# Kernel optimization log

Hardware: AMD Instinct MI355X
Metric: run time of the kernel (lower is better)

## Reference

```python
import jax, jax.numpy as jnp
import numpy as np

N = 100000


def seg_mean(feat, src, dst, n):
    # gather at src, scatter-mean at dst (PyG mean aggr: 0 for isolated nodes)
    s = jax.ops.segment_sum(feat[src], dst, num_segments=n)
    cnt = jax.ops.segment_sum(jnp.ones((src.shape[0],), feat.dtype), dst, num_segments=n)
    return s / jnp.maximum(cnt, 1.0)[:, None]


def setup_inputs() -> dict:
    key = jax.random.key(0)
    ks = jax.random.split(key, 8)
    d_in, d_h = 64, 32
    E = 1_250_000
    inp = {
        "x": jax.random.normal(ks[0], (N, d_in), jnp.float32),
        "W1_pos": jax.random.normal(ks[1], (2 * d_in, d_h), jnp.float32) * 0.05,
        "b1_pos": jnp.zeros((d_h,), jnp.float32),
        "W1_neg": jax.random.normal(ks[2], (2 * d_in, d_h), jnp.float32) * 0.05,
        "b1_neg": jnp.zeros((d_h,), jnp.float32),
        "W2_pos": jax.random.normal(ks[3], (3 * d_h, d_h), jnp.float32) * 0.05,
        "b2_pos": jnp.zeros((d_h,), jnp.float32),
        "W2_neg": jax.random.normal(ks[4], (3 * d_h, d_h), jnp.float32) * 0.05,
        "b2_neg": jnp.zeros((d_h,), jnp.float32),
        "pos_edge_index": jax.random.randint(ks[5], (2, E), 0, N, jnp.int64),
        "neg_edge_index": jax.random.randint(ks[6], (2, E), 0, N, jnp.int64),
    }
    return inp


def reference(x, W1_pos, b1_pos, W1_neg, b1_neg, W2_pos, b2_pos, W2_neg, b2_neg,
              pos_edge_index, neg_edge_index):
    ps, pd = pos_edge_index[0], pos_edge_index[1]
    ns, nd = neg_edge_index[0], neg_edge_index[1]
    n = x.shape[0]

    # --- layer 1 (first_aggr=True) ---
    ap = seg_mean(x, ps, pd, n)          # [N, 64]
    an = seg_mean(x, ns, nd, n)
    out_p = jnp.concatenate([ap, x], -1) @ W1_pos + b1_pos   # [N, 32]
    out_n = jnp.concatenate([an, x], -1) @ W1_neg + b1_neg
    z = jnp.tanh(jnp.concatenate([out_p, out_n], -1))        # [N, 64]

    # --- layer 2 (first_aggr=False) ---
    d_h = out_p.shape[-1]
    zp, zn = z[:, :d_h], z[:, d_h:]
    out_p = jnp.concatenate([seg_mean(zp, ps, pd, n), seg_mean(zn, ns, nd, n), zp], -1) @ W2_pos + b2_pos
    out_n = jnp.concatenate([seg_mean(zn, ps, pd, n), seg_mean(zp, ns, nd, n), zn], -1) @ W2_neg + b2_neg
    z = jnp.tanh(jnp.concatenate([out_p, out_n], -1))
    return z
```

## Files before the change

### kernel.cpp

```cpp
#include <hip/hip_runtime.h>
#include <math.h>


typedef _Float16 h4 __attribute__((ext_vector_type(4)));
typedef _Float16 h8 __attribute__((ext_vector_type(8)));
typedef float f32x4 __attribute__((ext_vector_type(4)));

__device__ inline h8 shflx8(h8 v, int m) {
    int4 i = __builtin_bit_cast(int4, v);
    i.x = __shfl_xor(i.x, m);
    i.y = __shfl_xor(i.y, m);
    i.z = __shfl_xor(i.z, m);
    i.w = __shfl_xor(i.w, m);
    return __builtin_bit_cast(h8, i);
}

__device__ inline float fast_tanh(float v) {
    float e = __expf(2.0f * v);
    return 1.0f - 2.0f / (e + 1.0f);
}


#define BSHIFT 9
#define BSIZE  512
#define NBMAX  512
#define NREP   8
#define RCAP   1024
#define CAP    (NREP * RCAP)
#define MAXPER 4992


__device__ inline float b1map(const float* W1p, const float* W1n, int k, int c)
{
    if (c < 32) {
        if (k < 64)   return W1p[k * 32 + c];
        if (k >= 128) return W1p[(k - 64) * 32 + c];
        return 0.0f;
    } else {
        int cn = c - 32;
        if (k >= 64)  return W1n[(k - 64) * 32 + cn];
        return 0.0f;
    }
}

__device__ inline float b2map(const float* W2p, const float* W2n, int k, int c)
{
    if (c < 32) {
        if (k < 32)               return W2p[k * 32 + c];
        if (k >= 96 && k < 128)   return W2p[(k - 96 + 32) * 32 + c];
        if (k >= 128 && k < 160)  return W2p[(k - 128 + 64) * 32 + c];
        return 0.0f;
    } else {
        int cn = c - 32;
        if (k >= 32 && k < 64)    return W2n[(k - 32) * 32 + cn];
        if (k >= 64 && k < 96)    return W2n[(k - 64 + 32) * 32 + cn];
        if (k >= 160)             return W2n[(k - 160 + 64) * 32 + cn];
        return 0.0f;
    }
}


__global__ void __launch_bounds__(256) mega_k(
    const int* __restrict__ pos, const int* __restrict__ neg,
    int* __restrict__ pcntR, unsigned* __restrict__ ebuf,
    int E, int n, int nb, int bblocks,
    const float4* __restrict__ x, h4* __restrict__ xh, int n4, int cvtBlocks,
    const float* __restrict__ W1p, const float* __restrict__ W1n,
    const float* __restrict__ W2p, const float* __restrict__ W2n,
    _Float16* __restrict__ Bpack)
{
    int tid = threadIdx.x;
    int bid = blockIdx.x;

    if (bid >= bblocks) {
        int cb = bid - bblocks;
        if (cb < cvtBlocks) {
            int gs = cvtBlocks * 256;
            for (int i = cb * 256 + tid; i < n4; i += gs) {
                float4 v = x[i];
                h4 o = { (_Float16)v.x, (_Float16)v.y, (_Float16)v.z, (_Float16)v.w };
                xh[i] = o;
            }
        } else {
            int slot = (cb - cvtBlocks) * 256 + tid;
            if (slot < 2 * 24 * 64) {
                int mat  = slot / (24 * 64);
                int rem  = slot % (24 * 64);
                int fg   = rem / 64;
                int lane = rem % 64;
                int kk = fg >> 2, nt = fg & 3;
                int g = lane >> 4, m = lane & 15;
                _Float16* dst = Bpack + (size_t)slot * 8;
                int c = nt * 16 + m;
                #pragma unroll
                for (int j = 0; j < 8; ++j) {
                    int k = kk * 32 + g * 8 + j;
                    float v = mat ? b2map(W2p, W2n, k, c) : b1map(W1p, W1n, k, c);
                    dst[j] = (_Float16)v;
                }
            }
        }
        return;
    }

    __shared__ int cnt[NBMAX], gbase[NBMAX], lofs[NBMAX], sc2[256];
    __shared__ unsigned erec[MAXPER], sorted[MAXPER];
    __shared__ unsigned short ep[MAXPER], pd[MAXPER];
    int rep = bid & (NREP - 1);
    int per = (2 * E + bblocks - 1) / bblocks;
    int e0 = bid * per;
    int e1 = min(e0 + per, 2 * E);
    int cntloc = e1 - e0;

    for (int i = tid; i < nb; i += 256) cnt[i] = 0;
    __syncthreads();

    for (int e = e0 + tid; e < e1; e += 256) {
        int nd, sr;
        if (e < E) { nd = pos[E + e];                 sr = pos[e]; }
        else       { int ee = e - E; nd = n + neg[E + ee]; sr = neg[ee]; }
        int p = nd >> BSHIFT;
        int li = e - e0;
        erec[li] = ((unsigned)(nd & (BSIZE - 1)) << 17) | (unsigned)sr;
        ep[li] = (unsigned short)p;
        atomicAdd(&cnt[p], 1);
    }
    __syncthreads();
    for (int i = tid; i < nb; i += 256) {
        int c = cnt[i];
        gbase[i] = c ? atomicAdd(&pcntR[rep * NBMAX + i], c) : 0;
    }
    {
        int a0 = (2 * tid     < nb) ? cnt[2 * tid]     : 0;
        int a1 = (2 * tid + 1 < nb) ? cnt[2 * tid + 1] : 0;
        int s = a0 + a1;
        sc2[tid] = s;
        __syncthreads();
        for (int off = 1; off < 256; off <<= 1) {
            int t = (tid >= off) ? sc2[tid - off] : 0;
            __syncthreads();
            sc2[tid] += t;
            __syncthreads();
        }
        int excl = sc2[tid] - s;
        if (2 * tid     < nb) lofs[2 * tid]     = excl;
        if (2 * tid + 1 < nb) lofs[2 * tid + 1] = excl + a0;
    }
    __syncthreads();
    for (int i = tid; i < nb; i += 256) cnt[i] = 0;
    __syncthreads();
    for (int li = tid; li < cntloc; li += 256) {
        int p = ep[li];
        int r = atomicAdd(&cnt[p], 1);
        int idx = lofs[p] + r;
        sorted[idx] = erec[li];
        pd[idx] = (unsigned short)p;
    }
    __syncthreads();
    for (int t = tid; t < cntloc; t += 256) {
        int p = pd[t];
        int g = gbase[p] + (t - lofs[p]);
        if (g < RCAP)
            ebuf[(size_t)p * CAP + rep * RCAP + g] = sorted[t];
    }
}

__global__ void __launch_bounds__(1024) scatter_k(
    const unsigned* __restrict__ ebuf, const int* __restrict__ pcntR,
    int* __restrict__ cur, int* __restrict__ col, int n, int nb)
{
    __shared__ int lcnt[BSIZE], lbase[BSIZE], sc[256], bb[NBMAX], crp[NREP];
    __shared__ int lcol[CAP];
    int p = blockIdx.x;
    int tid = threadIdx.x;
    int n2 = 2 * n;
    int lo = p << BSHIFT;
    int nn = min(BSIZE, n2 - lo);
    const unsigned* bbuf = ebuf + (size_t)p * CAP;

    if (tid < NREP) crp[tid] = min(pcntR[tid * NBMAX + p], RCAP);

    {
        int a0 = 0, a1 = 0, s = 0;
        if (tid < 256) {
            #pragma unroll
            for (int r = 0; r < NREP; ++r) {
                if (2 * tid     < nb) a0 += min(pcntR[r * NBMAX + 2 * tid],     RCAP);
                if (2 * tid + 1 < nb) a1 += min(pcntR[r * NBMAX + 2 * tid + 1], RCAP);
            }
            s = a0 + a1;
            sc[tid] = s;
        }
        __syncthreads();
        for (int off = 1; off < 256; off <<= 1) {
            int t = (tid < 256 && tid >= off) ? sc[tid - off] : 0;
            __syncthreads();
            if (tid < 256) sc[tid] += t;
            __syncthreads();
        }
        if (tid < 256) {
            int excl = sc[tid] - s;
            bb[2 * tid]     = excl;
            bb[2 * tid + 1] = excl + a0;
        }
    }

    for (int i = tid; i < BSIZE; i += 1024) lcnt[i] = 0;
    __syncthreads();
    int cnttot = crp[0] + crp[1] + crp[2] + crp[3] +
                 crp[4] + crp[5] + crp[6] + crp[7];
    #pragma unroll
    for (int r = 0; r < NREP; ++r) {
        int c = crp[r];
        const unsigned* buf = bbuf + r * RCAP;
        for (int i = tid; i < c; i += 1024)
            atomicAdd(&lcnt[buf[i] >> 17], 1);
    }
    __syncthreads();
    {
        int a0 = 0, a1 = 0, s = 0;
        if (tid < 256) {
            a0 = lcnt[2 * tid]; a1 = lcnt[2 * tid + 1];
            s = a0 + a1;
            sc[tid] = s;
        }
        __syncthreads();
        for (int off = 1; off < 256; off <<= 1) {
            int t = (tid < 256 && tid >= off) ? sc[tid - off] : 0;
            __syncthreads();
            if (tid < 256) sc[tid] += t;
            __syncthreads();
        }
        if (tid < 256) {
            int excl = sc[tid] - s;
            lbase[2 * tid]     = excl;
            lbase[2 * tid + 1] = excl + a0;
        }
    }
    __syncthreads();
    int gb = bb[p];
    for (int i = tid; i < nn; i += 1024)
        cur[lo + i] = gb + lbase[i] + lcnt[i];
    __syncthreads();
    #pragma unroll
    for (int r = 0; r < NREP; ++r) {
        int c = crp[r];
        const unsigned* buf = bbuf + r * RCAP;
        for (int i = tid; i < c; i += 1024) {
            unsigned v = buf[i];
            int slot = atomicAdd(&lbase[v >> 17], 1);
            lcol[slot] = (int)(v & 0x1FFFFu);
        }
    }
    __syncthreads();
    for (int t = tid; t < cnttot; t += 1024)
        col[gb + t] = lcol[t];
}


__global__ void __launch_bounds__(256) agg_k(
    const h8* __restrict__ feat8,
    const int* __restrict__ cur, const int* __restrict__ col,
    h8* __restrict__ ag8, int n)
{
    int tid = threadIdx.x;
    int wave = tid >> 6, lane = tid & 63;
    int s = lane >> 2, f = lane & 3;
    int list = s >> 3;
    int sub = s & 7;

    int stride = gridDim.x * 4;
    for (int node = blockIdx.x * 4 + wave; node < n; node += stride) {
        int idx = list ? n + node : node;
        int r0 = idx ? cur[idx - 1] : 0;
        int r1 = cur[idx];

        h8 acc0 = {}, acc1 = {};
        #pragma unroll 2
        for (int it = r0 + sub; it < r1; it += 8) {
            unsigned srcb = (unsigned)col[it] * 8;
            acc0 = acc0 + feat8[srcb + f];
            acc1 = acc1 + feat8[srcb + 4 + f];
        }
        acc0 = acc0 + shflx8(acc0, 4);
        acc1 = acc1 + shflx8(acc1, 4);
        acc0 = acc0 + shflx8(acc0, 8);
        acc1 = acc1 + shflx8(acc1, 8);
        acc0 = acc0 + shflx8(acc0, 16);
        acc1 = acc1 + shflx8(acc1, 16);
        _Float16 inv = (_Float16)(1.0f / (float)max(r1 - r0, 1));
        h8 iv = { inv, inv, inv, inv, inv, inv, inv, inv };
        if (sub == 0) {
            ag8[(unsigned)(node * 16 + list * 8 + f)]     = acc0 * iv;
            ag8[(unsigned)(node * 16 + list * 8 + 4 + f)] = acc1 * iv;
        }
    }
}


#define ROWP 200

__device__ inline int nmap(int g, int r) {
    return 32 * (16 * (g >> 3) + (r >> 2)) + 4 * (g & 7) + (r & 3);
}

__global__ void __launch_bounds__(256) gemm_k(
    const h8* __restrict__ ag8, const h8* __restrict__ feat8,
    const h8* __restrict__ Bp,
    const float* __restrict__ bp, const float* __restrict__ bn,
    float* __restrict__ outf, _Float16* __restrict__ outh,
    int f32out, int n)
{
    __shared__ _Float16 A_lds[64 * ROWP];
    int tid = threadIdx.x;
    int bid = blockIdx.x;

    for (int ch = tid; ch < 64 * 24; ch += 256) {
        int r = ch / 24, p = ch % 24;
        int row = min(nmap(bid, r), n - 1);
        h8 v = (p < 16) ? ag8[(size_t)row * 16 + p]
                        : feat8[(size_t)row * 8 + (p - 16)];
        *(h8*)&A_lds[r * ROWP + p * 8] = v;
    }
    __syncthreads();

    int w = tid >> 6, lane = tid & 63;
    int m = lane & 15, g = lane >> 4;

    h8 a[6];
    #pragma unroll
    for (int kk = 0; kk < 6; ++kk)
        a[kk] = *(const h8*)&A_lds[(w * 16 + m) * ROWP + kk * 32 + g * 8];

    #pragma unroll
    for (int nt = 0; nt < 4; ++nt) {
        f32x4 acc = { 0.f, 0.f, 0.f, 0.f };
        #pragma unroll
        for (int kk = 0; kk < 6; ++kk) {
            h8 b = Bp[(kk * 4 + nt) * 64 + lane];
            acc = __builtin_amdgcn_mfma_f32_16x16x32_f16(a[kk], b, acc, 0, 0, 0);
        }
        int colc = nt * 16 + m;
        float bias = (colc < 32) ? bp[colc] : bn[colc - 32];
        #pragma unroll
        for (int reg = 0; reg < 4; ++reg) {
            int node = nmap(bid, w * 16 + g * 4 + reg);
            if (node < n) {
                float val = fast_tanh(acc[reg] + bias);
                if (f32out) outf[(size_t)node * 64 + colc] = val;
                else        outh[(size_t)node * 64 + colc] = (_Float16)val;
            }
        }
    }
}

extern "C" void kernel_launch(void* const* d_in, const int* in_sizes, int n_in,
                              void* d_out, int out_size, void* d_ws, size_t ws_size,
                              hipStream_t stream)
{
    const float* x   = (const float*)d_in[0];
    const float* W1p = (const float*)d_in[1];
    const float* b1p = (const float*)d_in[2];
    const float* W1n = (const float*)d_in[3];
    const float* b1n = (const float*)d_in[4];
    const float* W2p = (const float*)d_in[5];
    const float* b2p = (const float*)d_in[6];
    const float* W2n = (const float*)d_in[7];
    const float* b2n = (const float*)d_in[8];
    const int*   pos = (const int*)d_in[9];
    const int*   neg = (const int*)d_in[10];

    int n = in_sizes[0] / 64;
    int E = in_sizes[9] / 2;
    int n2 = 2 * n;
    int nb = (n2 + BSIZE - 1) / BSIZE;

    int*      pcntR = (int*)d_ws;
    int*      cur   = pcntR + NREP * NBMAX;
    int*      col   = cur + n2;
    _Float16* Bpack = (_Float16*)(col + 2 * (size_t)E);
    _Float16* xh    = Bpack + 2 * 24 * 64 * 8;
    unsigned* ebuf  = (unsigned*)(xh + (size_t)n * 64);
    _Float16* zh    = (_Float16*)ebuf;
    h8*       ag8   = (h8*)d_out;

    hipMemsetAsync(pcntR, 0, NREP * NBMAX * sizeof(int), stream);

    int bblocks = 512;
    int n4 = n * 16;
    int cvtBlocks = 512;

    mega_k<<<bblocks + cvtBlocks + 12, 256, 0, stream>>>(
        pos, neg, pcntR, ebuf, E, n, nb, bblocks,
        (const float4*)x, (h4*)xh, n4, cvtBlocks,
        W1p, W1n, W2p, W2n, Bpack);

    scatter_k<<<nb, 1024, 0, stream>>>(ebuf, pcntR, cur, col, n, nb);

    int ablocks = 2048;
    int gblocks = (n + 63) / 64 + 5;

    agg_k <<<ablocks, 256, 0, stream>>>((const h8*)xh, cur, col, ag8, n);
    gemm_k<<<gblocks, 256, 0, stream>>>(ag8, (const h8*)xh, (const h8*)Bpack,
                                        b1p, b1n, nullptr, zh, 0, n);

    agg_k <<<ablocks, 256, 0, stream>>>((const h8*)zh, cur, col, ag8, n);
    gemm_k<<<gblocks, 256, 0, stream>>>(ag8, (const h8*)zh,
                                        (const h8*)(Bpack + 24 * 64 * 8),
                                        b2p, b2n, (float*)d_out, nullptr, 1, n);
}
```

Baseline: 262.6 us.

## Merge graph build and per-layer agg+GEMM into cooperative persistent kernels

Replaces the memset, bucketing kernel and scatter kernel with one cooperative build kernel that uses grid-wide syncs between phases and processes edges in chunks. Each layer's aggregation and GEMM are merged into one cooperative kernel with a grid sync between them, and the GEMM reads self features straight from global memory instead of staging them in LDS. This removes several launches and the gaps between them. In exchange it adds grid-sync cost, limits the grid to occupancy-bounded persistent blocks, and uses smaller per-block edge chunks. It falls back to the old launch path if a cooperative launch fails.

```diff
diff --git a/kernel.cpp b/kernel.cpp
--- a/kernel.cpp
+++ b/kernel.cpp
@@ -1,6 +1,9 @@
 #include <hip/hip_runtime.h>
+#include <hip/hip_cooperative_groups.h>
 #include <math.h>
 
+
+namespace cg = cooperative_groups;
 
 typedef _Float16 h4 __attribute__((ext_vector_type(4)));
 typedef _Float16 h8 __attribute__((ext_vector_type(8)));
@@ -20,15 +23,14 @@
     return 1.0f - 2.0f / (e + 1.0f);
 }
 
-
 #define BSHIFT 9
 #define BSIZE  512
 #define NBMAX  512
 #define NREP   8
 #define RCAP   1024
 #define CAP    (NREP * RCAP)
-#define MAXPER 4992
-
+#define MAXPER_F 4992
+#define MAXPER_C 2560
 
 __device__ inline float b1map(const float* W1p, const float* W1n, int k, int c)
 {
@@ -56,6 +58,302 @@
         if (k >= 64 && k < 96)    return W2n[(k - 64 + 32) * 32 + cn];
         if (k >= 160)             return W2n[(k - 160 + 64) * 32 + cn];
         return 0.0f;
+    }
+}
+
+__device__ inline int nmap(int g, int r) {
+    return 32 * (16 * (g >> 3) + (r >> 2)) + 4 * (g & 7) + (r & 3);
+}
+
+#define ROWP 200
+
+
+__global__ void __launch_bounds__(256) build_k(
+    const int* __restrict__ pos, const int* __restrict__ neg,
+    int* __restrict__ pcntR, unsigned* __restrict__ ebuf,
+    int E, int n, int nb,
+    const float4* __restrict__ x, h4* __restrict__ xh, int n4,
+    const float* __restrict__ W1p, const float* __restrict__ W1n,
+    const float* __restrict__ W2p, const float* __restrict__ W2n,
+    _Float16* __restrict__ Bpack,
+    int* __restrict__ cur, int* __restrict__ col)
+{
+    __shared__ int lcnt[NBMAX], lgb[NBMAX], sc[256], bb[NBMAX], crp[NREP];
+    __shared__ int lcol[CAP / 2];
+    __shared__ int lcol2[CAP / 2];
+    unsigned* erec = (unsigned*)lcol;
+    unsigned* sorted = erec + MAXPER_C;
+    unsigned short* ep = (unsigned short*)(sorted + MAXPER_C);
+    unsigned short* pd = ep + MAXPER_C;
+
+    cg::grid_group grid = cg::this_grid();
+    int tid = threadIdx.x;
+    int bid = blockIdx.x;
+    int g = gridDim.x;
+    int n2 = 2 * n;
+
+    for (int i = bid * 256 + tid; i < NREP * NBMAX; i += g * 256)
+        pcntR[i] = 0;
+    grid.sync();
+
+    {
+        int rep = bid & (NREP - 1);
+        int per = (2 * E + g - 1) / g;
+        int e0 = bid * per;
+        int e1 = min(e0 + per, 2 * E);
+        for (int c0 = e0; c0 < e1; c0 += MAXPER_C) {
+            int c1 = min(c0 + MAXPER_C, e1);
+            int cl = c1 - c0;
+            for (int i = tid; i < nb; i += 256) lcnt[i] = 0;
+            __syncthreads();
+            for (int e = c0 + tid; e < c1; e += 256) {
+                int nd, sr;
+                if (e < E) { nd = pos[E + e];                 sr = pos[e]; }
+                else       { int ee = e - E; nd = n + neg[E + ee]; sr = neg[ee]; }
+                int p = nd >> BSHIFT;
+                int li = e - c0;
+                erec[li] = ((unsigned)(nd & (BSIZE - 1)) << 17) | (unsigned)sr;
+                ep[li] = (unsigned short)p;
+                atomicAdd(&lcnt[p], 1);
+            }
+            __syncthreads();
+            for (int i = tid; i < nb; i += 256) {
+                int c = lcnt[i];
+                lgb[i] = c ? atomicAdd(&pcntR[rep * NBMAX + i], c) : 0;
+            }
+            {
+                int a0 = (2 * tid     < nb) ? lcnt[2 * tid]     : 0;
+                int a1 = (2 * tid + 1 < nb) ? lcnt[2 * tid + 1] : 0;
+                int s = a0 + a1;
+                sc[tid] = s;
+                __syncthreads();
+                for (int off = 1; off < 256; off <<= 1) {
+                    int t = (tid >= off) ? sc[tid - off] : 0;
+                    __syncthreads();
+                    sc[tid] += t;
+                    __syncthreads();
+                }
+                int excl = sc[tid] - s;
+                if (2 * tid     < nb) bb[2 * tid]     = excl;
+                if (2 * tid + 1 < nb) bb[2 * tid + 1] = excl + a0;
+            }
+            __syncthreads();
+            for (int i = tid; i < nb; i += 256) lcnt[i] = 0;
+            __syncthreads();
+            for (int li = tid; li < cl; li += 256) {
+                int p = ep[li];
+                int r = atomicAdd(&lcnt[p], 1);
+                int idx = bb[p] + r;
+                sorted[idx] = erec[li];
+                pd[idx] = (unsigned short)p;
+            }
+            __syncthreads();
+            for (int t = tid; t < cl; t += 256) {
+                int p = pd[t];
+                int gg = lgb[p] + (t - bb[p]);
+                if (gg < RCAP)
+                    ebuf[(size_t)p * CAP + rep * RCAP + gg] = sorted[t];
+            }
+            __syncthreads();
+        }
+    }
+    grid.sync();
+
+    {
+        int a0 = 0, a1 = 0, s = 0;
+        #pragma unroll
+        for (int r = 0; r < NREP; ++r) {
+            if (2 * tid     < nb) a0 += min(pcntR[r * NBMAX + 2 * tid],     RCAP);
+            if (2 * tid + 1 < nb) a1 += min(pcntR[r * NBMAX + 2 * tid + 1], RCAP);
+        }
+        s = a0 + a1;
+        sc[tid] = s;
+        __syncthreads();
+        for (int off = 1; off < 256; off <<= 1) {
+            int t = (tid >= off) ? sc[tid - off] : 0;
+            __syncthreads();
+            sc[tid] += t;
+            __syncthreads();
+        }
+        int excl = sc[tid] - s;
+        if (2 * tid     < nb) bb[2 * tid]     = excl;
+        if (2 * tid + 1 < nb) bb[2 * tid + 1] = excl + a0;
+    }
+    __syncthreads();
+
+    int ncvt = (n4 + 4095) / 4096;
+    int ntask = nb + 12 + ncvt;
+    for (int task = bid; task < ntask; task += g) {
+        if (task < nb) {
+            int p = task;
+            int lo = p << BSHIFT;
+            int nn = min(BSIZE, n2 - lo);
+            const unsigned* bbuf = ebuf + (size_t)p * CAP;
+            __syncthreads();
+            if (tid < NREP) crp[tid] = min(pcntR[tid * NBMAX + p], RCAP);
+            for (int i = tid; i < BSIZE; i += 256) lcnt[i] = 0;
+            __syncthreads();
+            int cnttot = 0;
+            #pragma unroll
+            for (int r = 0; r < NREP; ++r) {
+                int c = crp[r];
+                cnttot += c;
+                const unsigned* buf = bbuf + r * RCAP;
+                for (int i = tid; i < c; i += 256)
+                    atomicAdd(&lcnt[buf[i] >> 17], 1);
+            }
+            __syncthreads();
+            {
+                int a0 = lcnt[2 * tid], a1 = lcnt[2 * tid + 1];
+                int s = a0 + a1;
+                sc[tid] = s;
+                __syncthreads();
+                for (int off = 1; off < 256; off <<= 1) {
+                    int t = (tid >= off) ? sc[tid - off] : 0;
+                    __syncthreads();
+                    sc[tid] += t;
+                    __syncthreads();
+                }
+                int excl = sc[tid] - s;
+                lgb[2 * tid]     = excl;
+                lgb[2 * tid + 1] = excl + a0;
+            }
+            __syncthreads();
+            int gb = bb[p];
+            for (int i = tid; i < nn; i += 256)
+                cur[lo + i] = gb + lgb[i] + lcnt[i];
+            __syncthreads();
+            int* lc = lcol;
+            #pragma unroll
+            for (int r = 0; r < NREP; ++r) {
+                int c = crp[r];
+                const unsigned* buf = bbuf + r * RCAP;
+                for (int i = tid; i < c; i += 256) {
+                    unsigned v = buf[i];
+                    int slot = atomicAdd(&lgb[v >> 17], 1);
+                    if (slot < CAP / 2) lc[slot] = (int)(v & 0x1FFFFu);
+                    else                lcol2[slot - CAP / 2] = (int)(v & 0x1FFFFu);
+                }
+            }
+            __syncthreads();
+            for (int t = tid; t < cnttot; t += 256)
+                col[gb + t] = (t < CAP / 2) ? lc[t] : lcol2[t - CAP / 2];
+            __syncthreads();
+        } else if (task < nb + 12) {
+            int slot = (task - nb) * 256 + tid;
+            if (slot < 2 * 24 * 64) {
+                int mat  = slot / (24 * 64);
+                int rem  = slot % (24 * 64);
+                int fg   = rem / 64;
+                int lane = rem % 64;
+                int kk = fg >> 2, nt = fg & 3;
+                int gq = lane >> 4, m = lane & 15;
+                _Float16* dst = Bpack + (size_t)slot * 8;
+                int c = nt * 16 + m;
+                #pragma unroll
+                for (int j = 0; j < 8; ++j) {
+                    int k = kk * 32 + gq * 8 + j;
+                    float v = mat ? b2map(W2p, W2n, k, c) : b1map(W1p, W1n, k, c);
+                    dst[j] = (_Float16)v;
+                }
+            }
+        } else {
+            int ct = task - nb - 12;
+            int i0 = ct * 4096;
+            int i1 = min(i0 + 4096, n4);
+            for (int i = i0 + tid; i < i1; i += 256) {
+                float4 v = x[i];
+                h4 o = { (_Float16)v.x, (_Float16)v.y, (_Float16)v.z, (_Float16)v.w };
+                xh[i] = o;
+            }
+        }
+    }
+}
+
+__global__ void __launch_bounds__(256, 8) layer_k(
+    const h8* __restrict__ feat8,
+    const int* __restrict__ cur, const int* __restrict__ col,
+    const h8* __restrict__ Bp,
+    const float* __restrict__ bp, const float* __restrict__ bn,
+    h8* __restrict__ ag8, float* __restrict__ outf, _Float16* __restrict__ outh,
+    int f32out, int n, int ntiles)
+{
+    __shared__ _Float16 A_lds[64 * 132];
+    cg::grid_group gridg = cg::this_grid();
+    int tid = threadIdx.x;
+    int wave = tid >> 6, lane = tid & 63;
+
+    {
+        int s = lane >> 2, f = lane & 3;
+        int list = s >> 3;
+        int sub = s & 7;
+        int stride = gridDim.x * 4;
+        for (int node = blockIdx.x * 4 + wave; node < n; node += stride) {
+            int idx = list ? n + node : node;
+            int r0 = idx ? cur[idx - 1] : 0;
+            int r1 = cur[idx];
+            h8 acc0 = {}, acc1 = {};
+            #pragma unroll 2
+            for (int it = r0 + sub; it < r1; it += 8) {
+                unsigned srcb = (unsigned)col[it] * 8;
+                acc0 = acc0 + feat8[srcb + f];
+                acc1 = acc1 + feat8[srcb + 4 + f];
+            }
+            acc0 = acc0 + shflx8(acc0, 4);
+            acc1 = acc1 + shflx8(acc1, 4);
+            acc0 = acc0 + shflx8(acc0, 8);
+            acc1 = acc1 + shflx8(acc1, 8);
+            acc0 = acc0 + shflx8(acc0, 16);
+            acc1 = acc1 + shflx8(acc1, 16);
+            _Float16 inv = (_Float16)(1.0f / (float)max(r1 - r0, 1));
+            h8 iv = { inv, inv, inv, inv, inv, inv, inv, inv };
+            if (sub == 0) {
+                ag8[(unsigned)(node * 16 + list * 8 + f)]     = acc0 * iv;
+                ag8[(unsigned)(node * 16 + list * 8 + 4 + f)] = acc1 * iv;
+            }
+        }
+    }
+    gridg.sync();
+
+    int w = wave;
+    int m = lane & 15, g4 = lane >> 4;
+    for (int t = blockIdx.x; t < ntiles; t += gridDim.x) {
+        __syncthreads();
+        for (int ch = tid; ch < 64 * 16; ch += 256) {
+            int r = ch >> 4, c = ch & 15;
+            int row = min(nmap(t, r), n - 1);
+            *(h8*)&A_lds[r * 132 + c * 8] = ag8[(size_t)row * 16 + c];
+        }
+        __syncthreads();
+
+        int rowm = min(nmap(t, w * 16 + m), n - 1);
+        h8 a[6];
+        #pragma unroll
+        for (int kk = 0; kk < 4; ++kk)
+            a[kk] = *(const h8*)&A_lds[(w * 16 + m) * 132 + kk * 32 + g4 * 8];
+        a[4] = feat8[(size_t)rowm * 8 + g4];
+        a[5] = feat8[(size_t)rowm * 8 + 4 + g4];
+
+        #pragma unroll
+        for (int nt = 0; nt < 4; ++nt) {
+            f32x4 acc = { 0.f, 0.f, 0.f, 0.f };
+            #pragma unroll
+            for (int kk = 0; kk < 6; ++kk) {
+                h8 b = Bp[(kk * 4 + nt) * 64 + lane];
+                acc = __builtin_amdgcn_mfma_f32_16x16x32_f16(a[kk], b, acc, 0, 0, 0);
+            }
+            int colc = nt * 16 + m;
+            float bias = (colc < 32) ? bp[colc] : bn[colc - 32];
+            #pragma unroll
+            for (int reg = 0; reg < 4; ++reg) {
+                int node = nmap(t, w * 16 + g4 * 4 + reg);
+                if (node < n) {
+                    float val = fast_tanh(acc[reg] + bias);
+                    if (f32out) outf[(size_t)node * 64 + colc] = val;
+                    else        outh[(size_t)node * 64 + colc] = (_Float16)val;
+                }
+            }
+        }
     }
 }
 
@@ -104,8 +402,8 @@
     }
 
     __shared__ int cnt[NBMAX], gbase[NBMAX], lofs[NBMAX], sc2[256];
-    __shared__ unsigned erec[MAXPER], sorted[MAXPER];
-    __shared__ unsigned short ep[MAXPER], pd[MAXPER];
+    __shared__ unsigned erec[MAXPER_F], sorted[MAXPER_F];
+    __shared__ unsigned short ep[MAXPER_F], pd[MAXPER_F];
     int rep = bid & (NREP - 1);
     int per = (2 * E + bblocks - 1) / bblocks;
     int e0 = bid * per;
@@ -114,7 +412,6 @@
 
     for (int i = tid; i < nb; i += 256) cnt[i] = 0;
     __syncthreads();
-
     for (int e = e0 + tid; e < e1; e += 256) {
         int nd, sr;
         if (e < E) { nd = pos[E + e];                 sr = pos[e]; }
@@ -179,7 +476,6 @@
     const unsigned* bbuf = ebuf + (size_t)p * CAP;
 
     if (tid < NREP) crp[tid] = min(pcntR[tid * NBMAX + p], RCAP);
-
     {
         int a0 = 0, a1 = 0, s = 0;
         if (tid < 256) {
@@ -204,7 +500,6 @@
             bb[2 * tid + 1] = excl + a0;
         }
     }
-
     for (int i = tid; i < BSIZE; i += 1024) lcnt[i] = 0;
     __syncthreads();
     int cnttot = crp[0] + crp[1] + crp[2] + crp[3] +
@@ -257,7 +552,6 @@
         col[gb + t] = lcol[t];
 }
 
-
 __global__ void __launch_bounds__(256) agg_k(
     const h8* __restrict__ feat8,
     const int* __restrict__ cur, const int* __restrict__ col,
@@ -268,13 +562,11 @@
     int s = lane >> 2, f = lane & 3;
     int list = s >> 3;
     int sub = s & 7;
-
     int stride = gridDim.x * 4;
     for (int node = blockIdx.x * 4 + wave; node < n; node += stride) {
         int idx = list ? n + node : node;
         int r0 = idx ? cur[idx - 1] : 0;
         int r1 = cur[idx];
-
         h8 acc0 = {}, acc1 = {};
         #pragma unroll 2
         for (int it = r0 + sub; it < r1; it += 8) {
@@ -297,13 +589,6 @@
     }
 }
 
-
-#define ROWP 200
-
-__device__ inline int nmap(int g, int r) {
-    return 32 * (16 * (g >> 3) + (r >> 2)) + 4 * (g & 7) + (r & 3);
-}
-
 __global__ void __launch_bounds__(256) gemm_k(
     const h8* __restrict__ ag8, const h8* __restrict__ feat8,
     const h8* __restrict__ Bp,
@@ -314,7 +599,6 @@
     __shared__ _Float16 A_lds[64 * ROWP];
     int tid = threadIdx.x;
     int bid = blockIdx.x;
-
     for (int ch = tid; ch < 64 * 24; ch += 256) {
         int r = ch / 24, p = ch % 24;
         int row = min(nmap(bid, r), n - 1);
@@ -323,15 +607,12 @@
         *(h8*)&A_lds[r * ROWP + p * 8] = v;
     }
     __syncthreads();
-
     int w = tid >> 6, lane = tid & 63;
     int m = lane & 15, g = lane >> 4;
-
     h8 a[6];
     #pragma unroll
     for (int kk = 0; kk < 6; ++kk)
         a[kk] = *(const h8*)&A_lds[(w * 16 + m) * ROWP + kk * 32 + g * 8];
-
     #pragma unroll
     for (int nt = 0; nt < 4; ++nt) {
         f32x4 acc = { 0.f, 0.f, 0.f, 0.f };
@@ -353,6 +634,7 @@
         }
     }
 }
+
 
 extern "C" void kernel_launch(void* const* d_in, const int* in_sizes, int n_in,
                               void* d_out, int out_size, void* d_ws, size_t ws_size,
@@ -384,28 +666,87 @@
     _Float16* zh    = (_Float16*)ebuf;
     h8*       ag8   = (h8*)d_out;
 
+    int n4 = n * 16;
+    int ntiles = ((n + 511) / 512) * 8;
+
+    bool coop = true;
+    int occB = 0, occL = 0;
+    if (hipOccupancyMaxActiveBlocksPerMultiprocessor(&occB, build_k, 256, 0) != hipSuccess ||
+        hipOccupancyMaxActiveBlocksPerMultiprocessor(&occL, layer_k, 256, 0) != hipSuccess ||
+        occB < 1 || occL < 1)
+        coop = false;
+
+    if (coop) {
+        int gB = min(1024, occB * 256);
+        int gL = min(2048, occL * 256);
+        const float4* x4 = (const float4*)x;
+        h4* xh4 = (h4*)xh;
+        void* bargs[] = { (void*)&pos, (void*)&neg, (void*)&pcntR, (void*)&ebuf,
+                          (void*)&E, (void*)&n, (void*)&nb,
+                          (void*)&x4, (void*)&xh4, (void*)&n4,
+                          (void*)&W1p, (void*)&W1n, (void*)&W2p, (void*)&W2n,
+                          (void*)&Bpack, (void*)&cur, (void*)&col };
+        if (hipLaunchCooperativeKernel(build_k, dim3(gB), dim3(256),
+                                       bargs, 0, stream) != hipSuccess) {
+            (void)hipGetLastError();
+            coop = false;
+        } else {
+            const h8* f1 = (const h8*)xh;
+            const h8* Bp1 = (const h8*)Bpack;
+            float* nof = nullptr;
+            _Float16* zh_ = zh;
+            int zero = 0, one = 1;
+            void* l1[] = { (void*)&f1, (void*)&cur, (void*)&col, (void*)&Bp1,
+                           (void*)&b1p, (void*)&b1n, (void*)&ag8,
+                           (void*)&nof, (void*)&zh_, (void*)&zero,
+                           (void*)&n, (void*)&ntiles };
+            if (hipLaunchCooperativeKernel(layer_k, dim3(gL), dim3(256),
+                                           l1, 0, stream) != hipSuccess) {
+                (void)hipGetLastError();
+                coop = false;
+            } else {
+                const h8* f2 = (const h8*)zh;
+                const h8* Bp2 = (const h8*)(Bpack + 24 * 64 * 8);
+                float* of = (float*)d_out;
+                _Float16* noh = nullptr;
+                void* l2[] = { (void*)&f2, (void*)&cur, (void*)&col, (void*)&Bp2,
+                               (void*)&b2p, (void*)&b2n, (void*)&ag8,
+                               (void*)&of, (void*)&noh, (void*)&one,
+                               (void*)&n, (void*)&ntiles };
+                if (hipLaunchCooperativeKernel(layer_k, dim3(gL), dim3(256),
+                                               l2, 0, stream) == hipSuccess)
+                    return;
+                (void)hipGetLastError();
+                agg_k <<<2048, 256, 0, stream>>>((const h8*)zh, cur, col, ag8, n);
+                gemm_k<<<ntiles, 256, 0, stream>>>(ag8, (const h8*)zh,
+                                                   (const h8*)(Bpack + 24 * 64 * 8),
+                                                   b2p, b2n, (float*)d_out, nullptr, 1, n);
+                return;
+            }
+            agg_k <<<2048, 256, 0, stream>>>((const h8*)xh, cur, col, ag8, n);
+            gemm_k<<<ntiles, 256, 0, stream>>>(ag8, (const h8*)xh, (const h8*)Bpack,
+                                               b1p, b1n, nullptr, zh, 0, n);
+            agg_k <<<2048, 256, 0, stream>>>((const h8*)zh, cur, col, ag8, n);
+            gemm_k<<<ntiles, 256, 0, stream>>>(ag8, (const h8*)zh,
+                                               (const h8*)(Bpack + 24 * 64 * 8),
+                                               b2p, b2n, (float*)d_out, nullptr, 1, n);
+            return;
+        }
+    }
+
     hipMemsetAsync(pcntR, 0, NREP * NBMAX * sizeof(int), stream);
-
     int bblocks = 512;
-    int n4 = n * 16;
     int cvtBlocks = 512;
-
     mega_k<<<bblocks + cvtBlocks + 12, 256, 0, stream>>>(
         pos, neg, pcntR, ebuf, E, n, nb, bblocks,
         (const float4*)x, (h4*)xh, n4, cvtBlocks,
         W1p, W1n, W2p, W2n, Bpack);
-
     scatter_k<<<nb, 1024, 0, stream>>>(ebuf, pcntR, cur, col, n, nb);
-
-    int ablocks = 2048;
-    int gblocks = (n + 63) / 64 + 5;
-
-    agg_k <<<ablocks, 256, 0, stream>>>((const h8*)xh, cur, col, ag8, n);
-    gemm_k<<<gblocks, 256, 0, stream>>>(ag8, (const h8*)xh, (const h8*)Bpack,
-                                        b1p, b1n, nullptr, zh, 0, n);
-
-    agg_k <<<ablocks, 256, 0, stream>>>((const h8*)zh, cur, col, ag8, n);
-    gemm_k<<<gblocks, 256, 0, stream>>>(ag8, (const h8*)zh,
-                                        (const h8*)(Bpack + 24 * 64 * 8),
-                                        b2p, b2n, (float*)d_out, nullptr, 1, n);
-}
+    agg_k <<<2048, 256, 0, stream>>>((const h8*)xh, cur, col, ag8, n);
+    gemm_k<<<ntiles, 256, 0, stream>>>(ag8, (const h8*)xh, (const h8*)Bpack,
+                                       b1p, b1n, nullptr, zh, 0, n);
+    agg_k <<<2048, 256, 0, stream>>>((const h8*)zh, cur, col, ag8, n);
+    gemm_k<<<ntiles, 256, 0, stream>>>(ag8, (const h8*)zh,
+                                       (const h8*)(Bpack + 24 * 64 * 8),
+                                       b2p, b2n, (float*)d_out, nullptr, 1, n);
+}
```

Result: slower. 748.9 us (+185.2%).

## Fuse per-layer aggregation and GEMM into one persistent kernel with grid barrier

Applied to the files above, without the earlier changes.

Merges agg_k and gemm_k into a single layer_k launch per layer. Blocks first do the neighbour-mean aggregation and write results with agent-scope atomic stores, then meet at a global atomic-counter barrier before doing the MFMA GEMM over node tiles in a grid-stride loop. The self-feature half of the A operand is now loaded straight from global memory into registers instead of being staged through LDS. The aim is to cut kernel launches and the gap between them, at the cost of relying on all 1536 blocks being co-resident (launch_bounds 256,7) and a spin-wait barrier that has a timeout fallback.

```diff
diff --git a/kernel.cpp b/kernel.cpp
--- a/kernel.cpp
+++ b/kernel.cpp
@@ -20,7 +20,6 @@
     return 1.0f - 2.0f / (e + 1.0f);
 }
 
-
 #define BSHIFT 9
 #define BSIZE  512
 #define NBMAX  512
@@ -28,7 +27,6 @@
 #define RCAP   1024
 #define CAP    (NREP * RCAP)
 #define MAXPER 4992
-
 
 __device__ inline float b1map(const float* W1p, const float* W1n, int k, int c)
 {
@@ -57,6 +55,10 @@
         if (k >= 160)             return W2n[(k - 160 + 64) * 32 + cn];
         return 0.0f;
     }
+}
+
+__device__ inline int nmap(int g, int r) {
+    return 32 * (16 * (g >> 3) + (r >> 2)) + 4 * (g & 7) + (r & 3);
 }
 
 
@@ -114,7 +116,6 @@
 
     for (int i = tid; i < nb; i += 256) cnt[i] = 0;
     __syncthreads();
-
     for (int e = e0 + tid; e < e1; e += 256) {
         int nd, sr;
         if (e < E) { nd = pos[E + e];                 sr = pos[e]; }
@@ -179,7 +180,6 @@
     const unsigned* bbuf = ebuf + (size_t)p * CAP;
 
     if (tid < NREP) crp[tid] = min(pcntR[tid * NBMAX + p], RCAP);
-
     {
         int a0 = 0, a1 = 0, s = 0;
         if (tid < 256) {
@@ -204,7 +204,6 @@
             bb[2 * tid + 1] = excl + a0;
         }
     }
-
     for (int i = tid; i < BSIZE; i += 1024) lcnt[i] = 0;
     __syncthreads();
     int cnttot = crp[0] + crp[1] + crp[2] + crp[3] +
@@ -258,101 +257,113 @@
 }
 
 
-__global__ void __launch_bounds__(256) agg_k(
+__global__ void __launch_bounds__(256, 7) layer_k(
     const h8* __restrict__ feat8,
     const int* __restrict__ cur, const int* __restrict__ col,
-    h8* __restrict__ ag8, int n)
-{
+    const h8* __restrict__ Bp,
+    const float* __restrict__ bp, const float* __restrict__ bn,
+    unsigned long long* __restrict__ ag64,
+    float* __restrict__ outf, _Float16* __restrict__ outh,
+    int f32out, int n, int ntiles, int* __restrict__ bar, int nblk)
+{
+    __shared__ _Float16 A_lds[64 * 132];
     int tid = threadIdx.x;
     int wave = tid >> 6, lane = tid & 63;
-    int s = lane >> 2, f = lane & 3;
-    int list = s >> 3;
-    int sub = s & 7;
-
-    int stride = gridDim.x * 4;
-    for (int node = blockIdx.x * 4 + wave; node < n; node += stride) {
-        int idx = list ? n + node : node;
-        int r0 = idx ? cur[idx - 1] : 0;
-        int r1 = cur[idx];
-
-        h8 acc0 = {}, acc1 = {};
-        #pragma unroll 2
-        for (int it = r0 + sub; it < r1; it += 8) {
-            unsigned srcb = (unsigned)col[it] * 8;
-            acc0 = acc0 + feat8[srcb + f];
-            acc1 = acc1 + feat8[srcb + 4 + f];
-        }
-        acc0 = acc0 + shflx8(acc0, 4);
-        acc1 = acc1 + shflx8(acc1, 4);
-        acc0 = acc0 + shflx8(acc0, 8);
-        acc1 = acc1 + shflx8(acc1, 8);
-        acc0 = acc0 + shflx8(acc0, 16);
-        acc1 = acc1 + shflx8(acc1, 16);
-        _Float16 inv = (_Float16)(1.0f / (float)max(r1 - r0, 1));
-        h8 iv = { inv, inv, inv, inv, inv, inv, inv, inv };
-        if (sub == 0) {
-            ag8[(unsigned)(node * 16 + list * 8 + f)]     = acc0 * iv;
-            ag8[(unsigned)(node * 16 + list * 8 + 4 + f)] = acc1 * iv;
-        }
-    }
-}
-
-
-#define ROWP 200
-
-__device__ inline int nmap(int g, int r) {
-    return 32 * (16 * (g >> 3) + (r >> 2)) + 4 * (g & 7) + (r & 3);
-}
-
-__global__ void __launch_bounds__(256) gemm_k(
-    const h8* __restrict__ ag8, const h8* __restrict__ feat8,
-    const h8* __restrict__ Bp,
-    const float* __restrict__ bp, const float* __restrict__ bn,
-    float* __restrict__ outf, _Float16* __restrict__ outh,
-    int f32out, int n)
-{
-    __shared__ _Float16 A_lds[64 * ROWP];
-    int tid = threadIdx.x;
-    int bid = blockIdx.x;
-
-    for (int ch = tid; ch < 64 * 24; ch += 256) {
-        int r = ch / 24, p = ch % 24;
-        int row = min(nmap(bid, r), n - 1);
-        h8 v = (p < 16) ? ag8[(size_t)row * 16 + p]
-                        : feat8[(size_t)row * 8 + (p - 16)];
-        *(h8*)&A_lds[r * ROWP + p * 8] = v;
-    }
-    __syncthreads();
-
-    int w = tid >> 6, lane = tid & 63;
-    int m = lane & 15, g = lane >> 4;
-
-    h8 a[6];
-    #pragma unroll
-    for (int kk = 0; kk < 6; ++kk)
-        a[kk] = *(const h8*)&A_lds[(w * 16 + m) * ROWP + kk * 32 + g * 8];
-
-    #pragma unroll
-    for (int nt = 0; nt < 4; ++nt) {
-        f32x4 acc = { 0.f, 0.f, 0.f, 0.f };
+
+    {
+        int s = lane >> 2, f = lane & 3;
+        int list = s >> 3;
+        int sub = s & 7;
+        int stride = gridDim.x * 4;
+        for (int node = blockIdx.x * 4 + wave; node < n; node += stride) {
+            int idx = list ? n + node : node;
+            int r0 = idx ? cur[idx - 1] : 0;
+            int r1 = cur[idx];
+            h8 acc0 = {}, acc1 = {};
+            #pragma unroll 2
+            for (int it = r0 + sub; it < r1; it += 8) {
+                unsigned srcb = (unsigned)col[it] * 8;
+                acc0 = acc0 + feat8[srcb + f];
+                acc1 = acc1 + feat8[srcb + 4 + f];
+            }
+            acc0 = acc0 + shflx8(acc0, 4);
+            acc1 = acc1 + shflx8(acc1, 4);
+            acc0 = acc0 + shflx8(acc0, 8);
+            acc1 = acc1 + shflx8(acc1, 8);
+            acc0 = acc0 + shflx8(acc0, 16);
+            acc1 = acc1 + shflx8(acc1, 16);
+            _Float16 inv = (_Float16)(1.0f / (float)max(r1 - r0, 1));
+            h8 iv = { inv, inv, inv, inv, inv, inv, inv, inv };
+            if (sub == 0) {
+                h8 v0 = acc0 * iv, v1 = acc1 * iv;
+                ulonglong2 u0 = __builtin_bit_cast(ulonglong2, v0);
+                ulonglong2 u1 = __builtin_bit_cast(ulonglong2, v1);
+                size_t b0 = (size_t)(unsigned)(node * 16 + list * 8 + f) * 2;
+                size_t b1 = (size_t)(unsigned)(node * 16 + list * 8 + 4 + f) * 2;
+                __hip_atomic_store(&ag64[b0],     u0.x, __ATOMIC_RELAXED, __HIP_MEMORY_SCOPE_AGENT);
+                __hip_atomic_store(&ag64[b0 + 1], u0.y, __ATOMIC_RELAXED, __HIP_MEMORY_SCOPE_AGENT);
+                __hip_atomic_store(&ag64[b1],     u1.x, __ATOMIC_RELAXED, __HIP_MEMORY_SCOPE_AGENT);
+                __hip_atomic_store(&ag64[b1 + 1], u1.y, __ATOMIC_RELAXED, __HIP_MEMORY_SCOPE_AGENT);
+            }
+        }
+    }
+
+    __syncthreads();
+    if (tid == 0) {
+        __hip_atomic_fetch_add(bar, 1, __ATOMIC_RELEASE, __HIP_MEMORY_SCOPE_AGENT);
+        long spins = 0;
+        while (__hip_atomic_load(bar, __ATOMIC_ACQUIRE, __HIP_MEMORY_SCOPE_AGENT) < nblk) {
+            __builtin_amdgcn_s_sleep(16);
+            if (++spins > (1L << 20)) break;
+        }
+    }
+    __syncthreads();
+
+    int m = lane & 15, g4 = lane >> 4;
+    for (int t = blockIdx.x; t < ntiles; t += gridDim.x) {
+        __syncthreads();
+        for (int ch = tid; ch < 64 * 16; ch += 256) {
+            int r = ch >> 4, c = ch & 15;
+            int row = min(nmap(t, r), n - 1);
+            size_t bi = ((size_t)row * 16 + c) * 2;
+            unsigned long long w0 = __hip_atomic_load(&ag64[bi],     __ATOMIC_RELAXED, __HIP_MEMORY_SCOPE_AGENT);
+            unsigned long long w1 = __hip_atomic_load(&ag64[bi + 1], __ATOMIC_RELAXED, __HIP_MEMORY_SCOPE_AGENT);
+            ulonglong2 u; u.x = w0; u.y = w1;
+            *(h8*)&A_lds[r * 132 + c * 8] = __builtin_bit_cast(h8, u);
+        }
+        __syncthreads();
+
+        int rowm = min(nmap(t, wave * 16 + m), n - 1);
+        h8 a[6];
         #pragma unroll
-        for (int kk = 0; kk < 6; ++kk) {
-            h8 b = Bp[(kk * 4 + nt) * 64 + lane];
-            acc = __builtin_amdgcn_mfma_f32_16x16x32_f16(a[kk], b, acc, 0, 0, 0);
-        }
-        int colc = nt * 16 + m;
-        float bias = (colc < 32) ? bp[colc] : bn[colc - 32];
+        for (int kk = 0; kk < 4; ++kk)
+            a[kk] = *(const h8*)&A_lds[(wave * 16 + m) * 132 + kk * 32 + g4 * 8];
+        a[4] = feat8[(size_t)rowm * 8 + g4];
+        a[5] = feat8[(size_t)rowm * 8 + 4 + g4];
+
         #pragma unroll
-        for (int reg = 0; reg < 4; ++reg) {
-            int node = nmap(bid, w * 16 + g * 4 + reg);
-            if (node < n) {
-                float val = fast_tanh(acc[reg] + bias);
-                if (f32out) outf[(size_t)node * 64 + colc] = val;
-                else        outh[(size_t)node * 64 + colc] = (_Float16)val;
-            }
-        }
-    }
-}
+        for (int nt = 0; nt < 4; ++nt) {
+            f32x4 acc = { 0.f, 0.f, 0.f, 0.f };
+            #pragma unroll
+            for (int kk = 0; kk < 6; ++kk) {
+                h8 b = Bp[(kk * 4 + nt) * 64 + lane];
+                acc = __builtin_amdgcn_mfma_f32_16x16x32_f16(a[kk], b, acc, 0, 0, 0);
+            }
+            int colc = nt * 16 + m;
+            float bias = (colc < 32) ? bp[colc] : bn[colc - 32];
+            #pragma unroll
+            for (int reg = 0; reg < 4; ++reg) {
+                int node = nmap(t, wave * 16 + g4 * 4 + reg);
+                if (node < n) {
+                    float val = fast_tanh(acc[reg] + bias);
+                    if (f32out) outf[(size_t)node * 64 + colc] = val;
+                    else        outh[(size_t)node * 64 + colc] = (_Float16)val;
+                }
+            }
+        }
+    }
+}
+
 
 extern "C" void kernel_launch(void* const* d_in, const int* in_sizes, int n_in,
                               void* d_out, int out_size, void* d_ws, size_t ws_size,
@@ -376,15 +387,16 @@
     int nb = (n2 + BSIZE - 1) / BSIZE;
 
     int*      pcntR = (int*)d_ws;
-    int*      cur   = pcntR + NREP * NBMAX;
+    int*      bar   = pcntR + NREP * NBMAX;
+    int*      cur   = bar + 8;
     int*      col   = cur + n2;
     _Float16* Bpack = (_Float16*)(col + 2 * (size_t)E);
     _Float16* xh    = Bpack + 2 * 24 * 64 * 8;
     unsigned* ebuf  = (unsigned*)(xh + (size_t)n * 64);
     _Float16* zh    = (_Float16*)ebuf;
-    h8*       ag8   = (h8*)d_out;
-
-    hipMemsetAsync(pcntR, 0, NREP * NBMAX * sizeof(int), stream);
+    unsigned long long* ag64 = (unsigned long long*)d_out;
+
+    hipMemsetAsync(pcntR, 0, (NREP * NBMAX + 8) * sizeof(int), stream);
 
     int bblocks = 512;
     int n4 = n * 16;
@@ -397,15 +409,16 @@
 
     scatter_k<<<nb, 1024, 0, stream>>>(ebuf, pcntR, cur, col, n, nb);
 
-    int ablocks = 2048;
-    int gblocks = (n + 63) / 64 + 5;
-
-    agg_k <<<ablocks, 256, 0, stream>>>((const h8*)xh, cur, col, ag8, n);
-    gemm_k<<<gblocks, 256, 0, stream>>>(ag8, (const h8*)xh, (const h8*)Bpack,
-                                        b1p, b1n, nullptr, zh, 0, n);
-
-    agg_k <<<ablocks, 256, 0, stream>>>((const h8*)zh, cur, col, ag8, n);
-    gemm_k<<<gblocks, 256, 0, stream>>>(ag8, (const h8*)zh,
-                                        (const h8*)(Bpack + 24 * 64 * 8),
-                                        b2p, b2n, (float*)d_out, nullptr, 1, n);
-}
+    int lblocks = 1536;
+    int ntiles = ((n + 511) / 512) * 8;
+
+    layer_k<<<lblocks, 256, 0, stream>>>((const h8*)xh, cur, col,
+                                         (const h8*)Bpack, b1p, b1n,
+                                         ag64, nullptr, zh, 0, n, ntiles,
+                                         bar + 0, lblocks);
+    layer_k<<<lblocks, 256, 0, stream>>>((const h8*)zh, cur, col,
+                                         (const h8*)(Bpack + 24 * 64 * 8),
+                                         b2p, b2n, ag64,
+                                         (float*)d_out, nullptr, 1, n, ntiles,
+                                         bar + 4, lblocks);
+}
```

New measurement: 868.4 us. 3.31x slower.
